# Kernel tuning notes

Hardware: AMD Instinct MI355X
Metric: run time of the kernel (lower is better)

## Reference

```python
import jax, jax.numpy as jnp
import numpy as np
from jax import lax

D_MODEL = 96; D_STATE = 16; D_INNER = 192; DT_RANK = 6; K = 4
BSZ = 2; HH = 64; WW = 64


def setup_inputs() -> dict:
    key = jax.random.key(0)
    ks = jax.random.split(key, 16)
    f = lambda k, shape, s=0.02: (jax.random.normal(k, shape) * s).astype(jnp.float32)
    P = DT_RANK + 2 * D_STATE
    return {
        "x": jax.random.normal(ks[0], (BSZ, HH, WW, D_MODEL), jnp.float32),
        "W_in": f(ks[1], (2 * D_INNER, D_MODEL)),
        "b_in": jnp.zeros((2 * D_INNER,), jnp.float32),
        "conv_w": f(ks[2], (D_INNER, 1, 3, 3)),
        "conv_b": jnp.zeros((D_INNER,), jnp.float32),
        "W_xp": f(ks[3], (K * P, K * D_INNER)),
        "b_xp": jnp.zeros((K * P,), jnp.float32),
        "W_dt": f(ks[4], (K * D_INNER, K * DT_RANK)),
        "b_dt": f(ks[5], (K * D_INNER,), 0.1),
        "A_log": jax.random.normal(ks[6], (K * D_INNER, D_STATE), jnp.float32),
        "D_skip": jnp.ones((K * D_INNER,), jnp.float32),
        "dt_bias": jax.random.normal(ks[7], (K * D_INNER,), jnp.float32),
        "W_out": f(ks[8], (D_MODEL, D_INNER)),
        "b_out": jnp.zeros((D_MODEL,), jnp.float32),
        "gamma": jnp.ones((D_INNER,), jnp.float32),
        "beta": jnp.zeros((D_INNER,), jnp.float32),
    }


def cross_scan(x):
    # x: (B, D, H, W) -> (B, 4, D, L); dirs: row-major, col-major, and their reverses
    B, D, H, W = x.shape
    L = H * W
    x0 = x.reshape(B, D, L)
    x1 = jnp.swapaxes(x, 2, 3).reshape(B, D, L)
    return jnp.stack([x0, x1, x0[..., ::-1], x1[..., ::-1]], axis=1)


def cross_merge(ys):
    # ys: (B, 4, D, H, W) -> (B, D, L); inverse of cross_scan, summed
    B, Kk, D, H, W = ys.shape
    L = H * W
    yf = ys.reshape(B, Kk, D, L)
    y02 = yf[:, 0] + yf[:, 2, :, ::-1]
    y13 = yf[:, 1] + yf[:, 3, :, ::-1]
    y13 = jnp.swapaxes(y13.reshape(B, D, W, H), 2, 3).reshape(B, D, L)
    return y02 + y13


def selective_scan(u, dt, A, Bm, Cm, D_skip, dt_bias):
    # u, dt: (B,K,Dv,L); A: (K,Dv,N); Bm, Cm: (B,K,N,L); D_skip, dt_bias: (K,Dv)
    # NOTE: torch code repeats Bm/Cm across Dv; we broadcast instead (same math).
    dt = jax.nn.softplus(dt + dt_bias[None, :, :, None])
    dt_l = jnp.moveaxis(dt, -1, 0)   # (L,B,K,Dv)
    u_l = jnp.moveaxis(u, -1, 0)     # (L,B,K,Dv)
    B_l = jnp.moveaxis(Bm, -1, 0)    # (L,B,K,N)
    C_l = jnp.moveaxis(Cm, -1, 0)    # (L,B,K,N)

    def step(h, inp):
        dt_t, u_t, b_t, c_t = inp
        dA = jnp.exp(dt_t[..., None] * A[None])                 # (B,K,Dv,N)
        dBu = (dt_t * u_t)[..., None] * b_t[:, :, None, :]      # (B,K,Dv,N)
        h = dA * h + dBu
        y = jnp.einsum('bkdn,bkn->bkd', h, c_t)
        return h, y

    h0 = jnp.zeros(u.shape[:3] + (A.shape[-1],), u.dtype)
    _, ys = lax.scan(step, h0, (dt_l, u_l, B_l, C_l))
    ys = jnp.moveaxis(ys, 0, -1)  # (B,K,Dv,L)
    return ys + u * D_skip[None, :, :, None]


def reference(x, W_in, b_in, conv_w, conv_b, W_xp, b_xp, W_dt, b_dt,
              A_log, D_skip, dt_bias, W_out, b_out, gamma, beta):
    B, H, W, _ = x.shape
    L = H * W
    xz = x @ W_in.T + b_in
    xx, z = jnp.split(xz, 2, axis=-1)
    z = jax.nn.silu(z)
    xc = jnp.transpose(xx, (0, 3, 1, 2))  # (B, D, H, W)
    xc = lax.conv_general_dilated(xc, conv_w, (1, 1), 'SAME',
                                  feature_group_count=D_INNER,
                                  dimension_numbers=('NCHW', 'OIHW', 'NCHW'))
    xc = jax.nn.silu(xc + conv_b[None, :, None, None])

    xs = cross_scan(xc)                      # (B, K, D, L)
    xs_flat = xs.reshape(B, K * D_INNER, L)

    x_dbl = jnp.einsum('bcl,pc->bpl', xs_flat, W_xp) + b_xp[None, :, None]
    x_dbl = x_dbl.reshape(B, K, DT_RANK + 2 * D_STATE, L)
    dts, Bm, Cm = jnp.split(x_dbl, [DT_RANK, DT_RANK + D_STATE], axis=2)
    dts = dts.reshape(B, K * DT_RANK, L)
    dts = jnp.einsum('brl,dr->bdl', dts, W_dt) + b_dt[None, :, None]

    A = -jnp.exp(A_log).reshape(K, D_INNER, D_STATE)
    u = xs_flat.reshape(B, K, D_INNER, L)
    dt = dts.reshape(B, K, D_INNER, L)
    ys = selective_scan(u, dt, A, Bm, Cm,
                        D_skip.reshape(K, D_INNER), dt_bias.reshape(K, D_INNER))

    y = cross_merge(ys.reshape(B, K, D_INNER, H, W))  # (B, D, L)
    y = jnp.transpose(y.reshape(B, D_INNER, H, W), (0, 2, 3, 1))

    mu = jnp.mean(y, axis=-1, keepdims=True)
    var = jnp.mean(jnp.square(y - mu), axis=-1, keepdims=True)
    y = (y - mu) * lax.rsqrt(var + 1e-5) * gamma + beta
    y = y * z
    return y @ W_out.T + b_out
```

## Files before the change

### kernel.cpp

```cpp
#include <hip/hip_runtime.h>
#include <cstdint>
#include <cstddef>


#define CHUNK 16
#define NCK   256
#define SPAN  32
#define NSP   8

#if __has_builtin(__builtin_amdgcn_exp2f)
#define EXP2(x) __builtin_amdgcn_exp2f(x)
#else
#define EXP2(x) exp2f(x)
#endif
#define LOG2E 1.44269504088896340736f
#define LN2   0.69314718055994530942f

typedef __attribute__((ext_vector_type(8))) short short8;
typedef __attribute__((ext_vector_type(8))) unsigned short ushort8;
typedef __attribute__((ext_vector_type(4))) float f32x4;

__device__ __forceinline__ float siluf(float x){ return x * (1.f/(1.f+__expf(-x))); }
__device__ __forceinline__ float softplus_fast(float v){
  float e  = EXP2(v*LOG2E);
  float sp = LN2*__log2f(1.f + e);
  return (v > 20.f) ? v : sp;
}
__device__ __forceinline__ unsigned short f2b(float f){
  uint32_t u = __float_as_uint(f);
  uint32_t r = (u + 0x7fffu + ((u>>16)&1u)) >> 16;
  return (unsigned short)r;
}
__device__ __forceinline__ short8 cast8(const float* p){
  float4 f0 = *(const float4*)p;
  float4 f1 = *(const float4*)(p+4);
  unsigned short t[8] = {f2b(f0.x),f2b(f0.y),f2b(f0.z),f2b(f0.w),
                         f2b(f1.x),f2b(f1.y),f2b(f1.z),f2b(f1.w)};
  return *(short8*)t;
}

__global__ __launch_bounds__(256) void k_pack(
    const float* __restrict__ Wxp, const float* __restrict__ Win,
    const float* __restrict__ Wout,
    unsigned short* __restrict__ Wf, unsigned short* __restrict__ Wfin,
    unsigned short* __restrict__ Wfout)
{
  int tid = blockIdx.x*256 + threadIdx.x;
  int lane = tid & 63;
  int n = lane & 15, q = lane >> 4;
  if (tid < 18432){
    int rest = tid >> 6;
    int pt = rest % 6; rest /= 6;
    int k32 = rest & 3; rest >>= 2;
    int kc = rest % 6; int ph = rest / 6;
    int p = ph*96 + pt*16 + n;
    int kbase = kc*128 + k32*32 + q*8;
    unsigned short v[8];
#pragma unroll
    for (int j = 0; j < 8; j++)
      v[j] = (p < 152) ? f2b(Wxp[(size_t)p*768 + kbase + j]) : (unsigned short)0;
    *(ushort8*)(Wf + (size_t)tid*8) = *(ushort8*)v;
  } else if (tid < 23040){
    int e = tid - 18432;
    int rest = e >> 6;
    int nt = rest % 24, k32 = rest / 24;
    int p = nt*16 + n;
    int kbase = k32*32 + q*8;
    unsigned short v[8];
#pragma unroll
    for (int j = 0; j < 8; j++) v[j] = f2b(Win[(size_t)p*96 + kbase + j]);
    *(ushort8*)(Wfin + (size_t)e*8) = *(ushort8*)v;
  } else if (tid < 25344){
    int e = tid - 23040;
    int rest = e >> 6;
    int nt = rest % 6, k32 = rest / 6;
    int p = nt*16 + n;
    int kbase = k32*32 + q*8;
    unsigned short v[8];
#pragma unroll
    for (int j = 0; j < 8; j++) v[j] = f2b(Wout[(size_t)p*192 + kbase + j]);
    *(ushort8*)(Wfout + (size_t)e*8) = *(ushort8*)v;
  }
}

__global__ __launch_bounds__(256) void k_gemm_in(
    const float* __restrict__ x, const unsigned short* __restrict__ Wfin,
    const float* __restrict__ bias, float* __restrict__ xx, float* __restrict__ zs)
{
  const int tid = threadIdx.x;
  const int lane = tid & 63, w = tid >> 6;
  const int m0 = blockIdx.x*32;
  const int n = lane & 15, q = lane >> 4;
  f32x4 acc[2][6] = {};
#pragma unroll
  for (int k32 = 0; k32 < 3; k32++){
    int kb = k32*32 + q*8;
    short8 a[2];
#pragma unroll
    for (int mf = 0; mf < 2; mf++)
      a[mf] = cast8(x + (size_t)(m0 + mf*16 + n)*96 + kb);
#pragma unroll
    for (int j = 0; j < 6; j++){
      int nt = w*6 + j;
      short8 bfr = *(const short8*)(Wfin + ((size_t)(k32*24 + nt)*64 + lane)*8);
#pragma unroll
      for (int mf = 0; mf < 2; mf++)
        acc[mf][j] = __builtin_amdgcn_mfma_f32_16x16x32_bf16(a[mf], bfr, acc[mf][j], 0, 0, 0);
    }
  }
#pragma unroll
  for (int mf = 0; mf < 2; mf++)
#pragma unroll
    for (int j = 0; j < 6; j++){
      int nn = w*96 + j*16 + n;
      float bv = bias[nn];
#pragma unroll
      for (int reg = 0; reg < 4; reg++){
        int l = m0 + mf*16 + q*4 + reg;
        float v = acc[mf][j][reg] + bv;
        if (nn < 192) xx[(size_t)l*192 + nn] = v;
        else          zs[(size_t)l*192 + (nn-192)] = siluf(v);
      }
    }
}

__global__ __launch_bounds__(256) void k_conv(
    const float* __restrict__ xx, const float* __restrict__ cw, const float* __restrict__ cb,
    float* __restrict__ xc,
    unsigned short* __restrict__ xcb, unsigned short* __restrict__ xcTb)
{
  int gid = blockIdx.x*256 + threadIdx.x;
  int c4 = gid % 48; int c = c4*4;
  int l = (gid/48) & 4095;
  int b = gid / (48*4096);
  int h = l >> 6, w = l & 63;
  float sx = 0.f, sy = 0.f, sz = 0.f, sw = 0.f;
#pragma unroll
  for (int kh = 0; kh < 3; kh++){
    int h2 = h + kh - 1;
    if ((unsigned)h2 >= 64u) continue;
#pragma unroll
    for (int kw = 0; kw < 3; kw++){
      int w2 = w + kw - 1;
      if ((unsigned)w2 >= 64u) continue;
      float4 v = *(const float4*)(xx + ((size_t)b*4096 + h2*64 + w2)*192 + c);
      int o = kh*3 + kw;
      sx = fmaf(v.x, cw[(c+0)*9 + o], sx);
      sy = fmaf(v.y, cw[(c+1)*9 + o], sy);
      sz = fmaf(v.z, cw[(c+2)*9 + o], sz);
      sw = fmaf(v.w, cw[(c+3)*9 + o], sw);
    }
  }
  float4 cbv = *(const float4*)(cb + c);
  float4 s;
  s.x = siluf(sx + cbv.x); s.y = siluf(sy + cbv.y);
  s.z = siluf(sz + cbv.z); s.w = siluf(sw + cbv.w);
  unsigned short sb[4] = {f2b(s.x), f2b(s.y), f2b(s.z), f2b(s.w)};
  size_t i0 = ((size_t)b*4096 + l)*192 + c;
  *(float4*)(xc + i0) = s;
  *(uint2*)(xcb + i0) = *(uint2*)sb;
  int tl = (l & 63)*64 + (l >> 6);
  *(uint2*)(xcTb + ((size_t)b*4096 + tl)*192 + c) = *(uint2*)sb;
}

__global__ __launch_bounds__(256) void k_gemm_xdbl(
    const unsigned short* __restrict__ xcb, const unsigned short* __restrict__ xcTb,
    const unsigned short* __restrict__ Wf, const float* __restrict__ bxp,
    float* __restrict__ xdbl, float* __restrict__ dts_c)
{
  __shared__ unsigned short Bsh[4*6*64*8];
  const int tid = threadIdx.x;
  const int lane = tid & 63, w = tid >> 6;
  const int wl = w & 1, wp = w >> 1;
  const int l0 = blockIdx.x*32, ph = blockIdx.y, b = blockIdx.z;
  const int n = lane & 15, q = lane >> 4;
  f32x4 acc[3] = {};
  const unsigned short* slab0 = Wf + (size_t)ph*6*12288;
  for (int kc = 0; kc < 6; kc++){
    __syncthreads();
    const ushort8* srcp = (const ushort8*)(slab0 + (size_t)kc*12288);
#pragma unroll
    for (int t = 0; t < 6; t++) ((ushort8*)Bsh)[tid + t*256] = srcp[tid + t*256];
    __syncthreads();
#pragma unroll
    for (int k32 = 0; k32 < 4; k32++){
      int kk = kc*128 + k32*32;
      int dir = kk/192; int ch = kk%192 + q*8;
      const unsigned short* sp = (dir & 1) ? xcTb : xcb;
      bool rev = (dir >= 2);
      int ls = l0 + wl*16 + n;
      int row = rev ? 4095 - ls : ls;
      short8 a = *(const short8*)(sp + ((size_t)b*4096 + row)*192 + ch);
#pragma unroll
      for (int j = 0; j < 3; j++){
        short8 bfr = *(const short8*)&Bsh[((size_t)(k32*6 + wp*3 + j)*64 + lane)*8];
        acc[j] = __builtin_amdgcn_mfma_f32_16x16x32_bf16(a, bfr, acc[j], 0, 0, 0);
      }
    }
  }
#pragma unroll
  for (int j = 0; j < 3; j++){
    int p = ph*96 + (wp*3+j)*16 + n;
    if (p < 152){
      int k = p/38, pp = p%38;
      int off = (pp < 6) ? pp : pp + 2;
      float bias = bxp[p];
#pragma unroll
      for (int reg = 0; reg < 4; reg++){
        int l = l0 + wl*16 + q*4 + reg;
        float val = acc[j][reg] + bias;
        xdbl[(((size_t)b*4 + k)*4096 + l)*48 + off] = val;
        if (pp < 6) dts_c[((size_t)b*4096 + l)*24 + k*6 + pp] = val;
      }
    }
  }
}

__global__ __launch_bounds__(256) void k_scanA(
    const float* __restrict__ xc, const float* __restrict__ xdbl,
    const float* __restrict__ dts_c,
    const float* __restrict__ A_log, const float* __restrict__ Wdt,
    const float* __restrict__ bdt, const float* __restrict__ dtbias,
    const float* __restrict__ Dskip,
    float* __restrict__ ylcs, float* __restrict__ sdtb, float* __restrict__ Sb)
{
  const int lane = threadIdx.x & 63;
  const int wid  = __builtin_amdgcn_readfirstlane(blockIdx.x*4 + (threadIdx.x >> 6));
  const int ck = wid & (NCK-1); const int g = wid / NCK;
  const int dblk = g % 3; const int bk = g / 3;
  const int k = bk & 3; const int b = bk >> 2;
  const int d = dblk*64 + lane; const int ch = k*192 + d;
  float An[16];
  {
    const float4* ap = (const float4*)(A_log + (size_t)ch*16);
#pragma unroll
    for (int i = 0; i < 4; i++){
      float4 t = ap[i];
      An[4*i+0] = -LOG2E*__expf(t.x); An[4*i+1] = -LOG2E*__expf(t.y);
      An[4*i+2] = -LOG2E*__expf(t.z); An[4*i+3] = -LOG2E*__expf(t.w);
    }
  }
  float Wr[24];
#pragma unroll
  for (int r = 0; r < 24; r++) Wr[r] = Wdt[(size_t)ch*24 + r];
  const float bsum = bdt[ch] + dtbias[ch];
  const float Dv = Dskip[ch];
  const int l0 = ck*CHUNK;
  const bool rev = (k >= 2);
  const int tr = k & 1;
  const int T0 = tr ? ((l0 & 63)*64 + (l0 >> 6)) : l0;
  const int rs = tr ? 64 : 1;
  const int row0 = rev ? 4095 - T0 : T0;
  const int rstep = (rev ? -rs : rs)*192;
  const float* up  = xc + ((size_t)b*4096 + row0)*192 + d;
  const float* qc  = dts_c + ((size_t)b*4096 + l0)*24;
  const float* xbc = xdbl + (((size_t)b*4 + k)*4096 + l0)*48;
  float* ylp = ylcs + ((((size_t)b*4 + k)*4096 + l0)*192 + d)*2;
  float h[16];
#pragma unroll
  for (int n = 0; n < 16; n++) h[n] = 0.f;
  float sdt = 0.f;
#pragma unroll 4
  for (int t = 0; t < CHUNK; t++){
    float u  = up[0];
    float4 B0 = *(const float4*)(xbc + 8);
    float4 B1 = *(const float4*)(xbc + 12);
    float4 B2 = *(const float4*)(xbc + 16);
    float4 B3 = *(const float4*)(xbc + 20);
    float4 C0 = *(const float4*)(xbc + 24);
    float4 C1 = *(const float4*)(xbc + 28);
    float4 C2 = *(const float4*)(xbc + 32);
    float4 C3 = *(const float4*)(xbc + 36);
    float Bv[16] = {B0.x,B0.y,B0.z,B0.w, B1.x,B1.y,B1.z,B1.w,
                    B2.x,B2.y,B2.z,B2.w, B3.x,B3.y,B3.z,B3.w};
    float Cv[16] = {C0.x,C0.y,C0.z,C0.w, C1.x,C1.y,C1.z,C1.w,
                    C2.x,C2.y,C2.z,C2.w, C3.x,C3.y,C3.z,C3.w};
    float4 q0 = *(const float4*)(qc);
    float4 q1 = *(const float4*)(qc + 4);
    float4 q2 = *(const float4*)(qc + 8);
    float4 q3 = *(const float4*)(qc + 12);
    float4 q4 = *(const float4*)(qc + 16);
    float4 q5 = *(const float4*)(qc + 20);
    float qv[24] = {q0.x,q0.y,q0.z,q0.w, q1.x,q1.y,q1.z,q1.w,
                    q2.x,q2.y,q2.z,q2.w, q3.x,q3.y,q3.z,q3.w,
                    q4.x,q4.y,q4.z,q4.w, q5.x,q5.y,q5.z,q5.w};
    float v0 = bsum, v1 = 0.f, v2 = 0.f, v3 = 0.f;
#pragma unroll
    for (int r = 0; r < 24; r += 4){
      v0 = fmaf(Wr[r+0], qv[r+0], v0);
      v1 = fmaf(Wr[r+1], qv[r+1], v1);
      v2 = fmaf(Wr[r+2], qv[r+2], v2);
      v3 = fmaf(Wr[r+3], qv[r+3], v3);
    }
    float dt = softplus_fast((v0+v1) + (v2+v3));
    float dtu = dt*u;
    sdt += dt;
    float y0 = u*Dv;
    float y1 = 0.f;
#pragma unroll
    for (int n = 0; n < 16; n += 2){
      float dA0 = EXP2(dt*An[n]);
      float dA1 = EXP2(dt*An[n+1]);
      h[n]   = fmaf(dA0, h[n],   dtu*Bv[n]);
      h[n+1] = fmaf(dA1, h[n+1], dtu*Bv[n+1]);
      y0 = fmaf(h[n],   Cv[n],   y0);
      y1 = fmaf(h[n+1], Cv[n+1], y1);
    }
    *(float2*)ylp = make_float2(y0 + y1, sdt);
    qc += 24; xbc += 48; up += rstep; ylp += 384;
  }
  size_t base = ((size_t)wid*16)*64 + lane;
  sdtb[(size_t)wid*64 + lane] = sdt;
#pragma unroll
  for (int n = 0; n < 16; n++) Sb[base + n*64] = h[n];
}

__global__ __launch_bounds__(256) void k_scanB1(
    const float* __restrict__ A_log, const float* __restrict__ sdtb,
    const float* __restrict__ Sb,
    float* __restrict__ H0loc, float* __restrict__ cloc,
    float* __restrict__ SpanS, float* __restrict__ SpanC)
{
  int tid = blockIdx.x*256 + threadIdx.x;
  int lane = tid & 63; int n = (tid >> 6) & 15;
  int span = (tid >> 10) & (NSP-1); int g = tid >> 13;
  int dblk = g % 3; int bk = g / 3; int k = bk & 3;
  int ch = k*192 + dblk*64 + lane;
  float An = -LOG2E*__expf(A_log[(size_t)ch*16 + n]);
  float h = 0.f, cs = 0.f;
  int wid0 = g*NCK + span*SPAN;
#pragma unroll 8
  for (int c = 0; c < SPAN; c++){
    size_t sidx = ((size_t)(wid0 + c))*64 + lane;
    size_t idx  = (((size_t)(wid0 + c)*16) + n)*64 + lane;
    H0loc[idx] = h;
    if (n == 0) cloc[sidx] = cs;
    float sd = sdtb[sidx];
    h = fmaf(EXP2(An*sd), h, Sb[idx]);
    cs += sd;
  }
  size_t sp = (size_t)(g*NSP + span);
  SpanS[(sp*16 + n)*64 + lane] = h;
  if (n == 0) SpanC[sp*64 + lane] = cs;
}

__global__ __launch_bounds__(64) void k_scanB2(
    const float* __restrict__ A_log, const float* __restrict__ SpanS,
    const float* __restrict__ SpanC, float* __restrict__ H0span)
{
  int tid = blockIdx.x*64 + threadIdx.x;
  int lane = tid & 63; int n = (tid >> 6) & 15; int g = tid >> 10;
  int dblk = g % 3; int bk = g / 3; int k = bk & 3;
  int ch = k*192 + dblk*64 + lane;
  float An = -LOG2E*__expf(A_log[(size_t)ch*16 + n]);
  float h = 0.f;
#pragma unroll
  for (int span = 0; span < NSP; span++){
    size_t sp = (size_t)(g*NSP + span);
    size_t idx = (sp*16 + n)*64 + lane;
    H0span[idx] = h;
    h = fmaf(EXP2(An*SpanC[sp*64 + lane]), h, SpanS[idx]);
  }
}

__global__ __launch_bounds__(256) void k_scanC(
    const float* __restrict__ xdbl, const float* __restrict__ A_log,
    const float* __restrict__ ylcs,
    const float* __restrict__ H0loc, const float* __restrict__ cloc,
    const float* __restrict__ H0span,
    float* __restrict__ ys)
{
  const int lane = threadIdx.x & 63;
  const int wid  = __builtin_amdgcn_readfirstlane(blockIdx.x*4 + (threadIdx.x >> 6));
  const int ck = wid & (NCK-1); const int g = wid / NCK;
  const int dblk = g % 3; const int bk = g / 3;
  const int k = bk & 3; const int b = bk >> 2;
  const int d = dblk*64 + lane; const int ch = k*192 + d;
  float An[16];
  {
    const float4* ap = (const float4*)(A_log + (size_t)ch*16);
#pragma unroll
    for (int i = 0; i < 4; i++){
      float4 t = ap[i];
      An[4*i+0] = -LOG2E*__expf(t.x); An[4*i+1] = -LOG2E*__expf(t.y);
      An[4*i+2] = -LOG2E*__expf(t.z); An[4*i+3] = -LOG2E*__expf(t.w);
    }
  }
  const int l0 = ck*CHUNK;
  const bool rev = (k >= 2);
  const int tr = k & 1;
  const int T0 = tr ? ((l0 & 63)*64 + (l0 >> 6)) : l0;
  const int rs = tr ? 64 : 1;
  const int row0 = rev ? 4095 - T0 : T0;
  const int rstep = (rev ? -rs : rs)*192;
  const float* xbc = xdbl + (((size_t)b*4 + k)*4096 + l0)*48;
  const float* ylp = ylcs + ((((size_t)b*4 + k)*4096 + l0)*192 + d)*2;
  float* ysp = ys + ((size_t)(k*2 + b))*4096*192 + (size_t)row0*192 + d;
  float h0r[16];
  {
    size_t base = ((size_t)wid*16)*64 + lane;
    float cl = cloc[(size_t)wid*64 + lane];
    size_t sp = (size_t)(g*NSP + (ck >> 5));
#pragma unroll
    for (int n = 0; n < 16; n++){
      float hs = H0span[(sp*16 + n)*64 + lane];
      h0r[n] = fmaf(EXP2(An[n]*cl), hs, H0loc[base + n*64]);
    }
  }
#pragma unroll 4
  for (int t = 0; t < CHUNK; t++){
    float2 yc = *(const float2*)ylp;
    float4 C0 = *(const float4*)(xbc + 24);
    float4 C1 = *(const float4*)(xbc + 28);
    float4 C2 = *(const float4*)(xbc + 32);
    float4 C3 = *(const float4*)(xbc + 36);
    float Cv[16] = {C0.x,C0.y,C0.z,C0.w, C1.x,C1.y,C1.z,C1.w,
                    C2.x,C2.y,C2.z,C2.w, C3.x,C3.y,C3.z,C3.w};
    float cs = yc.y;
    float y0 = yc.x, y1 = 0.f;
#pragma unroll
    for (int n = 0; n < 16; n += 2){
      float e0 = EXP2(An[n]*cs)   * h0r[n];
      float e1 = EXP2(An[n+1]*cs) * h0r[n+1];
      y0 = fmaf(Cv[n],   e0, y0);
      y1 = fmaf(Cv[n+1], e1, y1);
    }
    ysp[0] = y0 + y1;
    ylp += 384; xbc += 48; ysp += rstep;
  }
}

__global__ __launch_bounds__(256) void k_lngemm(
    const float* __restrict__ ys, const float* __restrict__ zs,
    const float* __restrict__ gamma, const float* __restrict__ beta,
    const unsigned short* __restrict__ Wfout, const float* __restrict__ bout,
    float* __restrict__ out)
{
  __shared__ unsigned short Ash[32*200];
  const int tid = threadIdx.x;
  {
    const int row_l = tid >> 3, o = tid & 7;
    const int row = blockIdx.x*32 + row_l;
    const int b = row >> 12, l = row & 4095;
    const int c0 = o*24;
    float s[24];
#pragma unroll
    for (int j = 0; j < 6; j++){
      float sx = 0.f, sy = 0.f, sz = 0.f, sw = 0.f;
#pragma unroll
      for (int k = 0; k < 4; k++){
        float4 t = *(const float4*)(ys + (((size_t)(k*2+b))*4096 + l)*192 + c0 + j*4);
        sx += t.x; sy += t.y; sz += t.z; sw += t.w;
      }
      s[j*4+0]=sx; s[j*4+1]=sy; s[j*4+2]=sz; s[j*4+3]=sw;
    }
    float tot = 0.f;
#pragma unroll
    for (int j = 0; j < 24; j++) tot += s[j];
#pragma unroll
    for (int off = 1; off < 8; off <<= 1) tot += __shfl_xor(tot, off);
    float mean = tot*(1.f/192.f);
    float vs = 0.f;
#pragma unroll
    for (int j = 0; j < 24; j++){ s[j] -= mean; vs = fmaf(s[j], s[j], vs); }
#pragma unroll
    for (int off = 1; off < 8; off <<= 1) vs += __shfl_xor(vs, off);
    float rstd = rsqrtf(vs*(1.f/192.f) + 1e-5f);
    unsigned short vb[24];
#pragma unroll
    for (int j = 0; j < 6; j++){
      float4 g4 = *(const float4*)(gamma + c0 + j*4);
      float4 b4 = *(const float4*)(beta  + c0 + j*4);
      float4 z4 = *(const float4*)(zs + (size_t)row*192 + c0 + j*4);
      vb[j*4+0] = f2b((s[j*4+0]*rstd*g4.x + b4.x)*z4.x);
      vb[j*4+1] = f2b((s[j*4+1]*rstd*g4.y + b4.y)*z4.y);
      vb[j*4+2] = f2b((s[j*4+2]*rstd*g4.z + b4.z)*z4.z);
      vb[j*4+3] = f2b((s[j*4+3]*rstd*g4.w + b4.w)*z4.w);
    }
#pragma unroll
    for (int j = 0; j < 3; j++)
      *(ushort8*)(Ash + row_l*200 + c0 + j*8) = *(ushort8*)(vb + j*8);
  }
  __syncthreads();
  const int lane = tid & 63, w = tid >> 6;
  const int wm = w & 1, wn = w >> 1;
  const int n = lane & 15, q = lane >> 4;
  const int m0 = blockIdx.x*32 + wm*16;
  f32x4 acc[3] = {};
#pragma unroll
  for (int k32 = 0; k32 < 6; k32++){
    int kb = k32*32 + q*8;
    short8 a = *(const short8*)(Ash + (wm*16 + n)*200 + kb);
#pragma unroll
    for (int j = 0; j < 3; j++){
      int nt = wn*3 + j;
      short8 bfr = *(const short8*)(Wfout + ((size_t)(k32*6 + nt)*64 + lane)*8);
      acc[j] = __builtin_amdgcn_mfma_f32_16x16x32_bf16(a, bfr, acc[j], 0, 0, 0);
    }
  }
#pragma unroll
  for (int j = 0; j < 3; j++){
    int nn = wn*48 + j*16 + n;
    float bv = bout[nn];
#pragma unroll
    for (int reg = 0; reg < 4; reg++){
      int m = m0 + q*4 + reg;
      out[(size_t)m*96 + nn] = acc[j][reg] + bv;
    }
  }
}

extern "C" void kernel_launch(void* const* d_in, const int* in_sizes, int n_in,
                              void* d_out, int out_size, void* d_ws, size_t ws_size,
                              hipStream_t stream)
{
  const float* x      = (const float*)d_in[0];
  const float* W_in   = (const float*)d_in[1];
  const float* b_in   = (const float*)d_in[2];
  const float* conv_w = (const float*)d_in[3];
  const float* conv_b = (const float*)d_in[4];
  const float* W_xp   = (const float*)d_in[5];
  const float* b_xp   = (const float*)d_in[6];
  const float* W_dt   = (const float*)d_in[7];
  const float* b_dt   = (const float*)d_in[8];
  const float* A_log  = (const float*)d_in[9];
  const float* D_skip = (const float*)d_in[10];
  const float* dt_bias= (const float*)d_in[11];
  const float* W_out  = (const float*)d_in[12];
  const float* b_out  = (const float*)d_in[13];
  const float* gamma  = (const float*)d_in[14];
  const float* beta   = (const float*)d_in[15];
  float* out = (float*)d_out;

  float* ws     = (float*)d_ws;
  float* xx     = ws;
  float* zs     = ws + 1572864;
  float* xc     = ws + 3145728;
  float* xdbl   = ws + 4718592;
  float* ysb    = ws + 6291456;
  float* Sb     = ws + 12582912;
  float* H0loc  = ws + 18874368;
  float* sdtb   = ws + 25165824;
  float* dts_c  = ws + 25559040;
  float* ylcs   = ws + 25755648;
  float* cloc   = ws + 38338560;
  float* SpanS  = ws + 38731776;
  float* SpanC  = ws + 38928384;
  float* H0span = ws + 38940672;
  unsigned short* xcb   = (unsigned short*)(ws + 39137280);
  unsigned short* xcTb  = xcb + 1572864;
  unsigned short* Wf    = (unsigned short*)(ws + 40710144);
  unsigned short* Wfin  = (unsigned short*)(ws + 40783872);
  unsigned short* Wfout = (unsigned short*)(ws + 40802304);

  k_pack     <<<99,              256, 0, stream>>>(W_xp, W_in, W_out, Wf, Wfin, Wfout);
  k_gemm_in  <<<256,             256, 0, stream>>>(x, Wfin, b_in, xx, zs);
  k_conv     <<<1536,            256, 0, stream>>>(xx, conv_w, conv_b, xc, xcb, xcTb);
  k_gemm_xdbl<<<dim3(128, 2, 2), 256, 0, stream>>>(xcb, xcTb, Wf, b_xp, xdbl, dts_c);
  k_scanA    <<<1536,            256, 0, stream>>>(xc, xdbl, dts_c, A_log, W_dt, b_dt, dt_bias, D_skip, ylcs, sdtb, Sb);
  k_scanB1   <<<768,             256, 0, stream>>>(A_log, sdtb, Sb, H0loc, cloc, SpanS, SpanC);
  k_scanB2   <<<384,             64,  0, stream>>>(A_log, SpanS, SpanC, H0span);
  k_scanC    <<<1536,            256, 0, stream>>>(xdbl, A_log, ylcs, H0loc, cloc, H0span, ysb);
  k_lngemm   <<<256,             256, 0, stream>>>(ysb, zs, gamma, beta, Wfout, b_out, out);
}
```

Baseline: 210.1 us.

## Enlarge xdbl GEMM M-tile and repack scan intermediates for wider vector access

The x_dbl GEMM now computes two 16-row M tiles per wave, so each block covers 64 sequence positions and each staged weight fragment feeds twice as many MFMAs. The grid is halved to match. The per-chunk scan intermediates are changed in three ways: the local y and cumulative-dt values are packed as pairs of timesteps into float4 stores, and the chunk states (Sb, H0loc, H0span, SpanS) switch from n-major to n-contiguous per channel, so scanA and scanC can use float4 accesses. The aims are fewer memory transactions and better weight reuse, at the cost of fewer GEMM blocks and possibly less coalesced access in scanB1/B2.

After: 208.8 us. Within noise of the previous version (-0.6%).

```diff
diff --git a/kernel.cpp b/kernel.cpp
--- a/kernel.cpp
+++ b/kernel.cpp
@@ -172,9 +172,9 @@
   const int tid = threadIdx.x;
   const int lane = tid & 63, w = tid >> 6;
   const int wl = w & 1, wp = w >> 1;
-  const int l0 = blockIdx.x*32, ph = blockIdx.y, b = blockIdx.z;
+  const int l0 = blockIdx.x*64, ph = blockIdx.y, b = blockIdx.z;
   const int n = lane & 15, q = lane >> 4;
-  f32x4 acc[3] = {};
+  f32x4 acc[2][3] = {};
   const unsigned short* slab0 = Wf + (size_t)ph*6*12288;
   for (int kc = 0; kc < 6; kc++){
     __syncthreads();
@@ -188,32 +188,40 @@
       int dir = kk/192; int ch = kk%192 + q*8;
       const unsigned short* sp = (dir & 1) ? xcTb : xcb;
       bool rev = (dir >= 2);
-      int ls = l0 + wl*16 + n;
-      int row = rev ? 4095 - ls : ls;
-      short8 a = *(const short8*)(sp + ((size_t)b*4096 + row)*192 + ch);
+      short8 a[2];
+#pragma unroll
+      for (int mt = 0; mt < 2; mt++){
+        int ls = l0 + wl*32 + mt*16 + n;
+        int row = rev ? 4095 - ls : ls;
+        a[mt] = *(const short8*)(sp + ((size_t)b*4096 + row)*192 + ch);
+      }
 #pragma unroll
       for (int j = 0; j < 3; j++){
         short8 bfr = *(const short8*)&Bsh[((size_t)(k32*6 + wp*3 + j)*64 + lane)*8];
-        acc[j] = __builtin_amdgcn_mfma_f32_16x16x32_bf16(a, bfr, acc[j], 0, 0, 0);
-      }
-    }
-  }
-#pragma unroll
-  for (int j = 0; j < 3; j++){
-    int p = ph*96 + (wp*3+j)*16 + n;
-    if (p < 152){
-      int k = p/38, pp = p%38;
-      int off = (pp < 6) ? pp : pp + 2;
-      float bias = bxp[p];
-#pragma unroll
-      for (int reg = 0; reg < 4; reg++){
-        int l = l0 + wl*16 + q*4 + reg;
-        float val = acc[j][reg] + bias;
-        xdbl[(((size_t)b*4 + k)*4096 + l)*48 + off] = val;
-        if (pp < 6) dts_c[((size_t)b*4096 + l)*24 + k*6 + pp] = val;
-      }
-    }
-  }
+#pragma unroll
+        for (int mt = 0; mt < 2; mt++)
+          acc[mt][j] = __builtin_amdgcn_mfma_f32_16x16x32_bf16(a[mt], bfr, acc[mt][j], 0, 0, 0);
+      }
+    }
+  }
+#pragma unroll
+  for (int mt = 0; mt < 2; mt++)
+#pragma unroll
+    for (int j = 0; j < 3; j++){
+      int p = ph*96 + (wp*3+j)*16 + n;
+      if (p < 152){
+        int k = p/38, pp = p%38;
+        int off = (pp < 6) ? pp : pp + 2;
+        float bias = bxp[p];
+#pragma unroll
+        for (int reg = 0; reg < 4; reg++){
+          int l = l0 + wl*32 + mt*16 + q*4 + reg;
+          float val = acc[mt][j][reg] + bias;
+          xdbl[(((size_t)b*4 + k)*4096 + l)*48 + off] = val;
+          if (pp < 6) dts_c[((size_t)b*4096 + l)*24 + k*6 + pp] = val;
+        }
+      }
+    }
 }
 
 __global__ __launch_bounds__(256) void k_scanA(
@@ -255,64 +263,72 @@
   const float* up  = xc + ((size_t)b*4096 + row0)*192 + d;
   const float* qc  = dts_c + ((size_t)b*4096 + l0)*24;
   const float* xbc = xdbl + (((size_t)b*4 + k)*4096 + l0)*48;
-  float* ylp = ylcs + ((((size_t)b*4 + k)*4096 + l0)*192 + d)*2;
+  float* ylp = ylcs + ((((size_t)b*4 + k)*2048 + (size_t)ck*(CHUNK/2))*192 + d)*4;
   float h[16];
 #pragma unroll
   for (int n = 0; n < 16; n++) h[n] = 0.f;
   float sdt = 0.f;
 #pragma unroll 4
-  for (int t = 0; t < CHUNK; t++){
-    float u  = up[0];
-    float4 B0 = *(const float4*)(xbc + 8);
-    float4 B1 = *(const float4*)(xbc + 12);
-    float4 B2 = *(const float4*)(xbc + 16);
-    float4 B3 = *(const float4*)(xbc + 20);
-    float4 C0 = *(const float4*)(xbc + 24);
-    float4 C1 = *(const float4*)(xbc + 28);
-    float4 C2 = *(const float4*)(xbc + 32);
-    float4 C3 = *(const float4*)(xbc + 36);
-    float Bv[16] = {B0.x,B0.y,B0.z,B0.w, B1.x,B1.y,B1.z,B1.w,
-                    B2.x,B2.y,B2.z,B2.w, B3.x,B3.y,B3.z,B3.w};
-    float Cv[16] = {C0.x,C0.y,C0.z,C0.w, C1.x,C1.y,C1.z,C1.w,
-                    C2.x,C2.y,C2.z,C2.w, C3.x,C3.y,C3.z,C3.w};
-    float4 q0 = *(const float4*)(qc);
-    float4 q1 = *(const float4*)(qc + 4);
-    float4 q2 = *(const float4*)(qc + 8);
-    float4 q3 = *(const float4*)(qc + 12);
-    float4 q4 = *(const float4*)(qc + 16);
-    float4 q5 = *(const float4*)(qc + 20);
-    float qv[24] = {q0.x,q0.y,q0.z,q0.w, q1.x,q1.y,q1.z,q1.w,
-                    q2.x,q2.y,q2.z,q2.w, q3.x,q3.y,q3.z,q3.w,
-                    q4.x,q4.y,q4.z,q4.w, q5.x,q5.y,q5.z,q5.w};
-    float v0 = bsum, v1 = 0.f, v2 = 0.f, v3 = 0.f;
-#pragma unroll
-    for (int r = 0; r < 24; r += 4){
-      v0 = fmaf(Wr[r+0], qv[r+0], v0);
-      v1 = fmaf(Wr[r+1], qv[r+1], v1);
-      v2 = fmaf(Wr[r+2], qv[r+2], v2);
-      v3 = fmaf(Wr[r+3], qv[r+3], v3);
-    }
-    float dt = softplus_fast((v0+v1) + (v2+v3));
-    float dtu = dt*u;
-    sdt += dt;
-    float y0 = u*Dv;
-    float y1 = 0.f;
-#pragma unroll
-    for (int n = 0; n < 16; n += 2){
-      float dA0 = EXP2(dt*An[n]);
-      float dA1 = EXP2(dt*An[n+1]);
-      h[n]   = fmaf(dA0, h[n],   dtu*Bv[n]);
-      h[n+1] = fmaf(dA1, h[n+1], dtu*Bv[n+1]);
-      y0 = fmaf(h[n],   Cv[n],   y0);
-      y1 = fmaf(h[n+1], Cv[n+1], y1);
-    }
-    *(float2*)ylp = make_float2(y0 + y1, sdt);
-    qc += 24; xbc += 48; up += rstep; ylp += 384;
-  }
-  size_t base = ((size_t)wid*16)*64 + lane;
-  sdtb[(size_t)wid*64 + lane] = sdt;
-#pragma unroll
-  for (int n = 0; n < 16; n++) Sb[base + n*64] = h[n];
+  for (int tp = 0; tp < CHUNK/2; tp++){
+    float y2[2], cs2[2];
+#pragma unroll
+    for (int e = 0; e < 2; e++){
+      float u  = up[0];
+      float4 B0 = *(const float4*)(xbc + 8);
+      float4 B1 = *(const float4*)(xbc + 12);
+      float4 B2 = *(const float4*)(xbc + 16);
+      float4 B3 = *(const float4*)(xbc + 20);
+      float4 C0 = *(const float4*)(xbc + 24);
+      float4 C1 = *(const float4*)(xbc + 28);
+      float4 C2 = *(const float4*)(xbc + 32);
+      float4 C3 = *(const float4*)(xbc + 36);
+      float Bv[16] = {B0.x,B0.y,B0.z,B0.w, B1.x,B1.y,B1.z,B1.w,
+                      B2.x,B2.y,B2.z,B2.w, B3.x,B3.y,B3.z,B3.w};
+      float Cv[16] = {C0.x,C0.y,C0.z,C0.w, C1.x,C1.y,C1.z,C1.w,
+                      C2.x,C2.y,C2.z,C2.w, C3.x,C3.y,C3.z,C3.w};
+      float4 q0 = *(const float4*)(qc);
+      float4 q1 = *(const float4*)(qc + 4);
+      float4 q2 = *(const float4*)(qc + 8);
+      float4 q3 = *(const float4*)(qc + 12);
+      float4 q4 = *(const float4*)(qc + 16);
+      float4 q5 = *(const float4*)(qc + 20);
+      float qv[24] = {q0.x,q0.y,q0.z,q0.w, q1.x,q1.y,q1.z,q1.w,
+                      q2.x,q2.y,q2.z,q2.w, q3.x,q3.y,q3.z,q3.w,
+                      q4.x,q4.y,q4.z,q4.w, q5.x,q5.y,q5.z,q5.w};
+      float v0 = bsum, v1 = 0.f, v2 = 0.f, v3 = 0.f;
+#pragma unroll
+      for (int r = 0; r < 24; r += 4){
+        v0 = fmaf(Wr[r+0], qv[r+0], v0);
+        v1 = fmaf(Wr[r+1], qv[r+1], v1);
+        v2 = fmaf(Wr[r+2], qv[r+2], v2);
+        v3 = fmaf(Wr[r+3], qv[r+3], v3);
+      }
+      float dt = softplus_fast((v0+v1) + (v2+v3));
+      float dtu = dt*u;
+      sdt += dt;
+      float y0 = u*Dv;
+      float y1 = 0.f;
+#pragma unroll
+      for (int n = 0; n < 16; n += 2){
+        float dA0 = EXP2(dt*An[n]);
+        float dA1 = EXP2(dt*An[n+1]);
+        h[n]   = fmaf(dA0, h[n],   dtu*Bv[n]);
+        h[n+1] = fmaf(dA1, h[n+1], dtu*Bv[n+1]);
+        y0 = fmaf(h[n],   Cv[n],   y0);
+        y1 = fmaf(h[n+1], Cv[n+1], y1);
+      }
+      y2[e] = y0 + y1; cs2[e] = sdt;
+      qc += 24; xbc += 48; up += rstep;
+    }
+    *(float4*)ylp = make_float4(y2[0], cs2[0], y2[1], cs2[1]);
+    ylp += 768;
+  }
+  size_t rb = ((size_t)wid*64 + lane);
+  sdtb[rb] = sdt;
+  *(float4*)(Sb + rb*16 + 0)  = make_float4(h[0], h[1], h[2], h[3]);
+  *(float4*)(Sb + rb*16 + 4)  = make_float4(h[4], h[5], h[6], h[7]);
+  *(float4*)(Sb + rb*16 + 8)  = make_float4(h[8], h[9], h[10],h[11]);
+  *(float4*)(Sb + rb*16 + 12) = make_float4(h[12],h[13],h[14],h[15]);
 }
 
 __global__ __launch_bounds__(256) void k_scanB1(
@@ -322,7 +338,7 @@
     float* __restrict__ SpanS, float* __restrict__ SpanC)
 {
   int tid = blockIdx.x*256 + threadIdx.x;
-  int lane = tid & 63; int n = (tid >> 6) & 15;
+  int n = tid & 15; int lane = (tid >> 4) & 63;
   int span = (tid >> 10) & (NSP-1); int g = tid >> 13;
   int dblk = g % 3; int bk = g / 3; int k = bk & 3;
   int ch = k*192 + dblk*64 + lane;
@@ -331,17 +347,16 @@
   int wid0 = g*NCK + span*SPAN;
 #pragma unroll 8
   for (int c = 0; c < SPAN; c++){
-    size_t sidx = ((size_t)(wid0 + c))*64 + lane;
-    size_t idx  = (((size_t)(wid0 + c)*16) + n)*64 + lane;
-    H0loc[idx] = h;
-    if (n == 0) cloc[sidx] = cs;
-    float sd = sdtb[sidx];
-    h = fmaf(EXP2(An*sd), h, Sb[idx]);
+    size_t rb = ((size_t)(wid0 + c)*64 + lane);
+    H0loc[rb*16 + n] = h;
+    if (n == 0) cloc[rb] = cs;
+    float sd = sdtb[rb];
+    h = fmaf(EXP2(An*sd), h, Sb[rb*16 + n]);
     cs += sd;
   }
-  size_t sp = (size_t)(g*NSP + span);
-  SpanS[(sp*16 + n)*64 + lane] = h;
-  if (n == 0) SpanC[sp*64 + lane] = cs;
+  size_t sp = ((size_t)(g*NSP + span)*64 + lane);
+  SpanS[sp*16 + n] = h;
+  if (n == 0) SpanC[sp] = cs;
 }
 
 __global__ __launch_bounds__(64) void k_scanB2(
@@ -349,17 +364,16 @@
     const float* __restrict__ SpanC, float* __restrict__ H0span)
 {
   int tid = blockIdx.x*64 + threadIdx.x;
-  int lane = tid & 63; int n = (tid >> 6) & 15; int g = tid >> 10;
+  int n = tid & 15; int lane = (tid >> 4) & 63; int g = tid >> 10;
   int dblk = g % 3; int bk = g / 3; int k = bk & 3;
   int ch = k*192 + dblk*64 + lane;
   float An = -LOG2E*__expf(A_log[(size_t)ch*16 + n]);
   float h = 0.f;
 #pragma unroll
   for (int span = 0; span < NSP; span++){
-    size_t sp = (size_t)(g*NSP + span);
-    size_t idx = (sp*16 + n)*64 + lane;
-    H0span[idx] = h;
-    h = fmaf(EXP2(An*SpanC[sp*64 + lane]), h, SpanS[idx]);
+    size_t sp = ((size_t)(g*NSP + span)*64 + lane);
+    H0span[sp*16 + n] = h;
+    h = fmaf(EXP2(An*SpanC[sp]), h, SpanS[sp*16 + n]);
   }
 }
 
@@ -394,39 +408,48 @@
   const int row0 = rev ? 4095 - T0 : T0;
   const int rstep = (rev ? -rs : rs)*192;
   const float* xbc = xdbl + (((size_t)b*4 + k)*4096 + l0)*48;
-  const float* ylp = ylcs + ((((size_t)b*4 + k)*4096 + l0)*192 + d)*2;
+  const float* ylp = ylcs + ((((size_t)b*4 + k)*2048 + (size_t)ck*(CHUNK/2))*192 + d)*4;
   float* ysp = ys + ((size_t)(k*2 + b))*4096*192 + (size_t)row0*192 + d;
   float h0r[16];
   {
-    size_t base = ((size_t)wid*16)*64 + lane;
-    float cl = cloc[(size_t)wid*64 + lane];
-    size_t sp = (size_t)(g*NSP + (ck >> 5));
-#pragma unroll
-    for (int n = 0; n < 16; n++){
-      float hs = H0span[(sp*16 + n)*64 + lane];
-      h0r[n] = fmaf(EXP2(An[n]*cl), hs, H0loc[base + n*64]);
+    size_t rb = ((size_t)wid*64 + lane);
+    float cl = cloc[rb];
+    size_t sp = ((size_t)(g*NSP + (ck >> 5))*64 + lane);
+#pragma unroll
+    for (int i = 0; i < 4; i++){
+      float4 hl = *(const float4*)(H0loc + rb*16 + i*4);
+      float4 hs = *(const float4*)(H0span + sp*16 + i*4);
+      h0r[4*i+0] = fmaf(EXP2(An[4*i+0]*cl), hs.x, hl.x);
+      h0r[4*i+1] = fmaf(EXP2(An[4*i+1]*cl), hs.y, hl.y);
+      h0r[4*i+2] = fmaf(EXP2(An[4*i+2]*cl), hs.z, hl.z);
+      h0r[4*i+3] = fmaf(EXP2(An[4*i+3]*cl), hs.w, hl.w);
     }
   }
 #pragma unroll 4
-  for (int t = 0; t < CHUNK; t++){
-    float2 yc = *(const float2*)ylp;
-    float4 C0 = *(const float4*)(xbc + 24);
-    float4 C1 = *(const float4*)(xbc + 28);
-    float4 C2 = *(const float4*)(xbc + 32);
-    float4 C3 = *(const float4*)(xbc + 36);
-    float Cv[16] = {C0.x,C0.y,C0.z,C0.w, C1.x,C1.y,C1.z,C1.w,
-                    C2.x,C2.y,C2.z,C2.w, C3.x,C3.y,C3.z,C3.w};
-    float cs = yc.y;
-    float y0 = yc.x, y1 = 0.f;
-#pragma unroll
-    for (int n = 0; n < 16; n += 2){
-      float e0 = EXP2(An[n]*cs)   * h0r[n];
-      float e1 = EXP2(An[n+1]*cs) * h0r[n+1];
-      y0 = fmaf(Cv[n],   e0, y0);
-      y1 = fmaf(Cv[n+1], e1, y1);
-    }
-    ysp[0] = y0 + y1;
-    ylp += 384; xbc += 48; ysp += rstep;
+  for (int tp = 0; tp < CHUNK/2; tp++){
+    float4 yc = *(const float4*)ylp;
+#pragma unroll
+    for (int e = 0; e < 2; e++){
+      float yl = e ? yc.z : yc.x;
+      float cs = e ? yc.w : yc.y;
+      float4 C0 = *(const float4*)(xbc + 24);
+      float4 C1 = *(const float4*)(xbc + 28);
+      float4 C2 = *(const float4*)(xbc + 32);
+      float4 C3 = *(const float4*)(xbc + 36);
+      float Cv[16] = {C0.x,C0.y,C0.z,C0.w, C1.x,C1.y,C1.z,C1.w,
+                      C2.x,C2.y,C2.z,C2.w, C3.x,C3.y,C3.z,C3.w};
+      float y0 = yl, y1 = 0.f;
+#pragma unroll
+      for (int n = 0; n < 16; n += 2){
+        float e0 = EXP2(An[n]*cs)   * h0r[n];
+        float e1 = EXP2(An[n+1]*cs) * h0r[n+1];
+        y0 = fmaf(Cv[n],   e0, y0);
+        y1 = fmaf(Cv[n+1], e1, y1);
+      }
+      ysp[0] = y0 + y1;
+      xbc += 48; ysp += rstep;
+    }
+    ylp += 768;
   }
 }
 
@@ -553,13 +576,13 @@
   unsigned short* Wfin  = (unsigned short*)(ws + 40783872);
   unsigned short* Wfout = (unsigned short*)(ws + 40802304);
 
-  k_pack     <<<99,              256, 0, stream>>>(W_xp, W_in, W_out, Wf, Wfin, Wfout);
-  k_gemm_in  <<<256,             256, 0, stream>>>(x, Wfin, b_in, xx, zs);
-  k_conv     <<<1536,            256, 0, stream>>>(xx, conv_w, conv_b, xc, xcb, xcTb);
-  k_gemm_xdbl<<<dim3(128, 2, 2), 256, 0, stream>>>(xcb, xcTb, Wf, b_xp, xdbl, dts_c);
-  k_scanA    <<<1536,            256, 0, stream>>>(xc, xdbl, dts_c, A_log, W_dt, b_dt, dt_bias, D_skip, ylcs, sdtb, Sb);
-  k_scanB1   <<<768,             256, 0, stream>>>(A_log, sdtb, Sb, H0loc, cloc, SpanS, SpanC);
-  k_scanB2   <<<384,             64,  0, stream>>>(A_log, SpanS, SpanC, H0span);
-  k_scanC    <<<1536,            256, 0, stream>>>(xdbl, A_log, ylcs, H0loc, cloc, H0span, ysb);
-  k_lngemm   <<<256,             256, 0, stream>>>(ysb, zs, gamma, beta, Wfout, b_out, out);
-}
+  k_pack     <<<99,             256, 0, stream>>>(W_xp, W_in, W_out, Wf, Wfin, Wfout);
+  k_gemm_in  <<<256,            256, 0, stream>>>(x, Wfin, b_in, xx, zs);
+  k_conv     <<<1536,           256, 0, stream>>>(xx, conv_w, conv_b, xc, xcb, xcTb);
+  k_gemm_xdbl<<<dim3(64, 2, 2), 256, 0, stream>>>(xcb, xcTb, Wf, b_xp, xdbl, dts_c);
+  k_scanA    <<<1536,           256, 0, stream>>>(xc, xdbl, dts_c, A_log, W_dt, b_dt, dt_bias, D_skip, ylcs, sdtb, Sb);
+  k_scanB1   <<<768,            256, 0, stream>>>(A_log, sdtb, Sb, H0loc, cloc, SpanS, SpanC);
+  k_scanB2   <<<384,            64,  0, stream>>>(A_log, SpanS, SpanC, H0span);
+  k_scanC    <<<1536,           256, 0, stream>>>(xdbl, A_log, ylcs, H0loc, cloc, H0span, ysb);
+  k_lngemm   <<<256,            256, 0, stream>>>(ysb, zs, gamma, beta, Wfout, b_out, out);
+}
```
